# Kernel tuning notes

Measured on AMD Instinct MI355X. Metric: run time of the kernel, lower is better.

## Reference

```python
import jax, jax.numpy as jnp
import numpy as np

T, B, C, K, E = 1024, 32, 1024, 1024, 16  # seq, batch, d_model(=in=out), key_dim, n_experts
LOSS_SCALE = 0.01


def setup_inputs() -> dict:
    key0 = jax.random.key(0)
    k0, k1, k2, k3 = jax.random.split(key0, 4)
    x = jax.random.normal(k0, (T, B, C), dtype=jnp.float32)
    key = jax.random.normal(k1, (1, B, K), dtype=jnp.float32)
    bnd = float(np.sqrt(6.0 / (K + E)))  # xavier_uniform for assign Linear
    assign_w = jax.random.uniform(k2, (K, E), jnp.float32, -bnd, bnd)
    assign_b = jnp.zeros((E,), jnp.float32)
    a = float(np.sqrt(6.0) / (C + C))  # dynamic_init_method=1
    pw_w1 = jax.random.uniform(k3, (E, C * C), jnp.float32, -a, a)
    return {"x": x, "key": key, "assign_w": assign_w, "assign_b": assign_b, "pw_w1": pw_w1}


def reference(x, key, assign_w, assign_b, pw_w1):
    Tn, Bn, Cn = x.shape
    Tr = key.shape[0]  # key is provided -> Tr = 1 (one routing decision per batch element)
    En = assign_b.shape[0]
    # routing: softmax over experts (gumbel_tau=0 -> plain softmax branch)
    logits = key.reshape(Tr * Bn, -1) @ assign_w + assign_b  # (Tr*B, E)
    resp = jax.nn.softmax(logits, axis=-1)
    importance = resp.sum(axis=0)  # (E,)
    loss = LOSS_SCALE * jnp.std(importance, ddof=1) / jnp.mean(importance)  # torch.std is unbiased
    # mix expert weights: (Tr*B, E) @ (E, O*I) -> per-token/sentence weight matrix
    w = (resp @ pw_w1).reshape(Tr, Bn, Cn, Cn)  # (Tr, B, O, I)
    # batched matvec, broadcasting Tr=1 over T (sum over size-1 axis r == broadcast)
    y = jnp.einsum('rboi,tbi->tbo', w, x)
    return x + y, loss
```

## Files before the change

### kernel.cpp

```cpp
#include <hip/hip_runtime.h>
#include <stdint.h>


#define TBC   (1024*32*1024)

typedef __attribute__((ext_vector_type(8))) __bf16 bf16x8;
typedef __attribute__((ext_vector_type(4))) float  floatx4;

#define XSWZ(r) ((((r) & 3) ^ (((r) >> 2) & 3)))

__device__ __forceinline__ unsigned short f2bf(float f) {
  unsigned u = __float_as_uint(f);
  unsigned r = u + 0x7fffu + ((u >> 16) & 1u);
  return (unsigned short)(r >> 16);
}
__device__ __forceinline__ float bf2f(unsigned short u) {
  return __uint_as_float(((unsigned)u) << 16);
}

__device__ __forceinline__ void async16(const void* g, void* l) {
  __builtin_amdgcn_global_load_lds(
      (const __attribute__((address_space(1))) void*)(unsigned long long)(uintptr_t)g,
      (__attribute__((address_space(3))) void*)(unsigned int)(uintptr_t)l,
      16, 0, 0);
}

__global__ __launch_bounds__(256) void route_conv_kernel(
    const float* __restrict__ key, const float* __restrict__ aw,
    const float* __restrict__ ab, float* __restrict__ resp,
    const float4* __restrict__ x, ushort4* __restrict__ xb) {
  const int tid = threadIdx.x;
  if (blockIdx.x >= 32) {
    const int i0 = (blockIdx.x - 32) * 256 + tid;
    #pragma unroll
    for (int j = 0; j < 8; ++j) {
      const int i = i0 + j * 1048576;
      float4 v = x[i];
      ushort4 o;
      o.x = f2bf(v.x); o.y = f2bf(v.y); o.z = f2bf(v.z); o.w = f2bf(v.w);
      xb[i] = o;
    }
    return;
  }
  __shared__ float part[16][17];
  __shared__ float logit[16];
  const int b = blockIdx.x;
  const int e = tid & 15, ks = tid >> 4;
  const float* kb = key + b * 1024 + ks * 64;
  float acc = 0.f;
  #pragma unroll 8
  for (int k = 0; k < 64; ++k)
    acc = fmaf(kb[k], aw[(ks * 64 + k) * 16 + e], acc);
  part[e][ks] = acc;
  __syncthreads();
  if (tid < 16) {
    float s = ab[tid];
    #pragma unroll
    for (int j = 0; j < 16; ++j) s += part[tid][j];
    logit[tid] = s;
  }
  __syncthreads();
  if (tid < 16) {
    float m = logit[0];
    #pragma unroll
    for (int j = 1; j < 16; ++j) m = fmaxf(m, logit[j]);
    float s = 0.f;
    #pragma unroll
    for (int j = 0; j < 16; ++j) s += expf(logit[j] - m);
    resp[b * 16 + tid] = expf(logit[tid] - m) / s;
  }
}

__global__ __launch_bounds__(256, 4) void mix_loss_kernel(
    const float4* __restrict__ pw, const float* __restrict__ resp,
    ushort4* __restrict__ W, float* __restrict__ loss_out) {
  __shared__ float rs[512];
  const int tid = threadIdx.x;
  rs[tid] = resp[tid];
  rs[tid + 256] = resp[tid + 256];
  __syncthreads();
  if (blockIdx.x == 0 && tid == 0) {
    float imp[16];
    float mu = 0.f;
    #pragma unroll
    for (int e = 0; e < 16; ++e) {
      float s = 0.f;
      for (int bb = 0; bb < 32; ++bb) s += rs[bb * 16 + e];
      imp[e] = s; mu += s;
    }
    mu *= (1.f / 16.f);
    float var = 0.f;
    #pragma unroll
    for (int e = 0; e < 16; ++e) { float d = imp[e] - mu; var += d * d; }
    var *= (1.f / 15.f);
    loss_out[0] = 0.01f * sqrtf(var) / mu;
  }
  const int p = blockIdx.x * 256 + tid;
  float4 v[16];
  #pragma unroll
  for (int e = 0; e < 16; ++e) v[e] = pw[e * 262144 + p];
  #pragma unroll
  for (int b = 0; b < 32; ++b) {
    float ax = 0.f, ay = 0.f, az = 0.f, aww = 0.f;
    #pragma unroll
    for (int e = 0; e < 16; ++e) {
      const float r = rs[b * 16 + e];
      ax = fmaf(r, v[e].x, ax); ay = fmaf(r, v[e].y, ay);
      az = fmaf(r, v[e].z, az); aww = fmaf(r, v[e].w, aww);
    }
    ushort4 o;
    o.x = f2bf(ax); o.y = f2bf(ay); o.z = f2bf(az); o.w = f2bf(aww);
    W[(size_t)b * 262144 + p] = o;
  }
}

__global__ __launch_bounds__(512, 2) void gemm_kernel(
    const unsigned short* __restrict__ xb,
    const unsigned short* __restrict__ Wb,
    float* __restrict__ out) {
  __shared__ unsigned short lds[4][2][8192];
  const int tid  = threadIdx.x;
  const int lane = tid & 63;
  const int wave = tid >> 6;
  const int wm = wave >> 2;
  const int wn = wave & 3;

  const int gid   = blockIdx.x;
  const int xcd   = gid & 7;
  const int local = gid >> 3;
  const int b     = xcd * 4 + (local >> 4);
  const int sub   = local & 15;
  const int t0    = (sub >> 2) * 256;
  const int o0    = (sub & 3) * 256;

  const unsigned short* gA[2];
  const unsigned short* gB[2];
  #pragma unroll
  for (int j = 0; j < 2; ++j) {
    const int s  = j * 512 + tid;
    const int r  = s >> 2;
    const int cg = (s & 3) ^ XSWZ(r);
    gA[j] = xb + (size_t)(t0 + r) * 32768 + (size_t)b * 1024 + cg * 8;
    gB[j] = Wb + (size_t)b * 1048576 + (size_t)(o0 + r) * 1024 + cg * 8;
  }

  floatx4 acc[8][4];
  #pragma unroll
  for (int a = 0; a < 8; ++a)
    #pragma unroll
    for (int ni = 0; ni < 4; ++ni)
      acc[a][ni] = floatx4{0.f, 0.f, 0.f, 0.f};

  auto stage = [&](int bufi) {
    #pragma unroll
    for (int j = 0; j < 2; ++j) {
      const int dst = (j * 512 + wave * 64) * 8;
      async16(gA[j], &lds[bufi][0][dst]);
      async16(gB[j], &lds[bufi][1][dst]);
      gA[j] += 32; gB[j] += 32;
    }
  };

  auto compute = [&](int bufi) {
    const unsigned short* lA = &lds[bufi][0][0];
    const unsigned short* lB = &lds[bufi][1][0];
    bf16x8 bfr[4];
    #pragma unroll
    for (int ni = 0; ni < 4; ++ni) {
      const int r = wn * 64 + ni * 16 + (lane & 15);
      const int slot = (lane >> 4) ^ XSWZ(r);
      bfr[ni] = *(const bf16x8*)(lB + r * 32 + slot * 8);
    }
    #pragma unroll
    for (int half = 0; half < 2; ++half) {
      bf16x8 afr[4];
      #pragma unroll
      for (int mi = 0; mi < 4; ++mi) {
        const int r = wm * 128 + half * 64 + mi * 16 + (lane & 15);
        const int slot = (lane >> 4) ^ XSWZ(r);
        afr[mi] = *(const bf16x8*)(lA + r * 32 + slot * 8);
      }
      __builtin_amdgcn_s_setprio(1);
      #pragma unroll
      for (int mi = 0; mi < 4; ++mi)
        #pragma unroll
        for (int ni = 0; ni < 4; ++ni)
          acc[half * 4 + mi][ni] = __builtin_amdgcn_mfma_f32_16x16x32_bf16(
              afr[mi], bfr[ni], acc[half * 4 + mi][ni], 0, 0, 0);
      __builtin_amdgcn_s_setprio(0);
      if (half == 0) __builtin_amdgcn_s_barrier();
    }
  };

  stage(0); stage(1); stage(2);

  for (int t = 0; t < 32; ++t) {
    if (t <= 28) {
      stage((t + 3) & 3);
      asm volatile("s_waitcnt vmcnt(12)" ::: "memory");
    } else if (t == 29) {
      asm volatile("s_waitcnt vmcnt(8)" ::: "memory");
    } else if (t == 30) {
      asm volatile("s_waitcnt vmcnt(4)" ::: "memory");
    } else {
      asm volatile("s_waitcnt vmcnt(0)" ::: "memory");
    }
    __builtin_amdgcn_s_barrier();
    asm volatile("" ::: "memory");
    compute(t & 3);
    asm volatile("s_waitcnt lgkmcnt(0)" ::: "memory");
    __builtin_amdgcn_s_barrier();
  }

  #pragma unroll
  for (int a = 0; a < 8; ++a) {
    const int tb = t0 + wm * 128 + (a >> 2) * 64 + (a & 3) * 16 + (lane >> 4) * 4;
    #pragma unroll
    for (int ni = 0; ni < 4; ++ni) {
      const int o = o0 + wn * 64 + ni * 16 + (lane & 15);
      #pragma unroll
      for (int v = 0; v < 4; ++v) {
        const size_t idx = (size_t)(tb + v) * 32768 + (size_t)b * 1024 + o;
        out[idx] = acc[a][ni][v] + bf2f(xb[idx]);
      }
    }
  }
}

extern "C" void kernel_launch(void* const* d_in, const int* in_sizes, int n_in,
                              void* d_out, int out_size, void* d_ws, size_t ws_size,
                              hipStream_t stream) {
  const float* x   = (const float*)d_in[0];
  const float* key = (const float*)d_in[1];
  const float* aw  = (const float*)d_in[2];
  const float* ab  = (const float*)d_in[3];
  const float* pw  = (const float*)d_in[4];
  float* out = (float*)d_out;

  char* ws = (char*)d_ws;
  unsigned short* Wb = (unsigned short*)ws;
  unsigned short* xb = (unsigned short*)(ws + 67108864);
  float* resp        = (float*)(ws + 134217728);

  route_conv_kernel<<<4128, 256, 0, stream>>>(key, aw, ab, resp,
                                              (const float4*)x, (ushort4*)xb);
  mix_loss_kernel<<<1024, 256, 0, stream>>>((const float4*)pw, resp,
                                            (ushort4*)Wb, out + TBC);
  gemm_kernel<<<512, 512, 0, stream>>>(xb, Wb, out);
}
```

Measured before the change: 402.9 us.

## Switch GEMM to BK=64 double-buffered pipeline with 8-way XOR swizzle

The GEMM K-tile grows from 32 to 64, and the pipeline goes from four 32-wide stages to two 64-wide buffers. That halves the number of loop iterations and barriers, drops the mid-compute barrier, and uses a new 8-slot XOR swizzle for the wider LDS rows. The conversion kernel now processes contiguous chunks of 4 float4 per thread over twice as many blocks. The mix kernel's launch bounds are relaxed to allow more registers. The cost is a shallower prefetch depth, which can expose more memory latency per iteration.

```diff
diff --git a/kernel.cpp b/kernel.cpp
--- a/kernel.cpp
+++ b/kernel.cpp
@@ -6,8 +6,6 @@
 
 typedef __attribute__((ext_vector_type(8))) __bf16 bf16x8;
 typedef __attribute__((ext_vector_type(4))) float  floatx4;
-
-#define XSWZ(r) ((((r) & 3) ^ (((r) >> 2) & 3)))
 
 __device__ __forceinline__ unsigned short f2bf(float f) {
   unsigned u = __float_as_uint(f);
@@ -31,10 +29,10 @@
     const float4* __restrict__ x, ushort4* __restrict__ xb) {
   const int tid = threadIdx.x;
   if (blockIdx.x >= 32) {
-    const int i0 = (blockIdx.x - 32) * 256 + tid;
-    #pragma unroll
-    for (int j = 0; j < 8; ++j) {
-      const int i = i0 + j * 1048576;
+    const int base = (blockIdx.x - 32) * 1024 + tid;
+    #pragma unroll
+    for (int j = 0; j < 4; ++j) {
+      const int i = base + j * 256;
       float4 v = x[i];
       ushort4 o;
       o.x = f2bf(v.x); o.y = f2bf(v.y); o.z = f2bf(v.z); o.w = f2bf(v.w);
@@ -71,7 +69,7 @@
   }
 }
 
-__global__ __launch_bounds__(256, 4) void mix_loss_kernel(
+__global__ __launch_bounds__(256, 2) void mix_loss_kernel(
     const float4* __restrict__ pw, const float* __restrict__ resp,
     ushort4* __restrict__ W, float* __restrict__ loss_out) {
   __shared__ float rs[512];
@@ -118,9 +116,11 @@
     const unsigned short* __restrict__ xb,
     const unsigned short* __restrict__ Wb,
     float* __restrict__ out) {
-  __shared__ unsigned short lds[4][2][8192];
+  __shared__ unsigned short lds[65536];
   const int tid  = threadIdx.x;
   const int lane = tid & 63;
+  const int ln15 = lane & 15;
+  const int hi   = lane >> 4;
   const int wave = tid >> 6;
   const int wm = wave >> 2;
   const int wn = wave & 3;
@@ -133,16 +133,17 @@
   const int t0    = (sub >> 2) * 256;
   const int o0    = (sub & 3) * 256;
 
-  const unsigned short* gA[2];
-  const unsigned short* gB[2];
-  #pragma unroll
-  for (int j = 0; j < 2; ++j) {
-    const int s  = j * 512 + tid;
-    const int r  = s >> 2;
-    const int cg = (s & 3) ^ XSWZ(r);
-    gA[j] = xb + (size_t)(t0 + r) * 32768 + (size_t)b * 1024 + cg * 8;
-    gB[j] = Wb + (size_t)b * 1048576 + (size_t)(o0 + r) * 1024 + cg * 8;
-  }
+  const unsigned short* src[2][2][2];
+  #pragma unroll
+  for (int h = 0; h < 2; ++h)
+    #pragma unroll
+    for (int s = 0; s < 2; ++s) {
+      const int G  = tid + 512 * s;
+      const int r  = G >> 3;
+      const int kg = (G & 7) ^ (r & 7);
+      src[0][h][s] = xb + (size_t)(t0 + h * 128 + r) * 32768 + (size_t)b * 1024 + kg * 8;
+      src[1][h][s] = Wb + (size_t)b * 1048576 + (size_t)(o0 + h * 128 + r) * 1024 + kg * 8;
+    }
 
   floatx4 acc[8][4];
   #pragma unroll
@@ -151,77 +152,76 @@
     for (int ni = 0; ni < 4; ++ni)
       acc[a][ni] = floatx4{0.f, 0.f, 0.f, 0.f};
 
-  auto stage = [&](int bufi) {
-    #pragma unroll
-    for (int j = 0; j < 2; ++j) {
-      const int dst = (j * 512 + wave * 64) * 8;
-      async16(gA[j], &lds[bufi][0][dst]);
-      async16(gB[j], &lds[bufi][1][dst]);
-      gA[j] += 32; gB[j] += 32;
-    }
+  auto stage = [&](int bufBase) {
+    #pragma unroll
+    for (int ab = 0; ab < 2; ++ab)
+      #pragma unroll
+      for (int h = 0; h < 2; ++h)
+        #pragma unroll
+        for (int s = 0; s < 2; ++s) {
+          async16(src[ab][h][s],
+                  lds + bufBase + ab * 16384 + h * 8192 + (wave * 64 + 512 * s) * 8);
+          src[ab][h][s] += 64;
+        }
   };
 
-  auto compute = [&](int bufi) {
-    const unsigned short* lA = &lds[bufi][0][0];
-    const unsigned short* lB = &lds[bufi][1][0];
-    bf16x8 bfr[4];
+  auto compute = [&](int bufBase) {
+    const unsigned short* LA = lds + bufBase + wm * 8192;
+    const unsigned short* LB = lds + bufBase + 16384 + (wn >> 1) * 8192;
+    bf16x8 Bf[4][2];
     #pragma unroll
     for (int ni = 0; ni < 4; ++ni) {
-      const int r = wn * 64 + ni * 16 + (lane & 15);
-      const int slot = (lane >> 4) ^ XSWZ(r);
-      bfr[ni] = *(const bf16x8*)(lB + r * 32 + slot * 8);
-    }
-    #pragma unroll
-    for (int half = 0; half < 2; ++half) {
-      bf16x8 afr[4];
+      const int r = (wn & 1) * 64 + ni * 16 + ln15;
+      #pragma unroll
+      for (int kk = 0; kk < 2; ++kk)
+        Bf[ni][kk] = *(const bf16x8*)(LB + r * 64 + (((kk * 4 + hi) ^ (r & 7)) * 8));
+    }
+    #pragma unroll
+    for (int qm = 0; qm < 2; ++qm) {
+      bf16x8 Af[4][2];
       #pragma unroll
       for (int mi = 0; mi < 4; ++mi) {
-        const int r = wm * 128 + half * 64 + mi * 16 + (lane & 15);
-        const int slot = (lane >> 4) ^ XSWZ(r);
-        afr[mi] = *(const bf16x8*)(lA + r * 32 + slot * 8);
+        const int r = (qm * 4 + mi) * 16 + ln15;
+        #pragma unroll
+        for (int kk = 0; kk < 2; ++kk)
+          Af[mi][kk] = *(const bf16x8*)(LA + r * 64 + (((kk * 4 + hi) ^ (r & 7)) * 8));
       }
       __builtin_amdgcn_s_setprio(1);
       #pragma unroll
       for (int mi = 0; mi < 4; ++mi)
         #pragma unroll
         for (int ni = 0; ni < 4; ++ni)
-          acc[half * 4 + mi][ni] = __builtin_amdgcn_mfma_f32_16x16x32_bf16(
-              afr[mi], bfr[ni], acc[half * 4 + mi][ni], 0, 0, 0);
+          #pragma unroll
+          for (int kk = 0; kk < 2; ++kk)
+            acc[qm * 4 + mi][ni] = __builtin_amdgcn_mfma_f32_16x16x32_bf16(
+                Af[mi][kk], Bf[ni][kk], acc[qm * 4 + mi][ni], 0, 0, 0);
       __builtin_amdgcn_s_setprio(0);
-      if (half == 0) __builtin_amdgcn_s_barrier();
     }
   };
 
-  stage(0); stage(1); stage(2);
-
-  for (int t = 0; t < 32; ++t) {
-    if (t <= 28) {
-      stage((t + 3) & 3);
-      asm volatile("s_waitcnt vmcnt(12)" ::: "memory");
-    } else if (t == 29) {
-      asm volatile("s_waitcnt vmcnt(8)" ::: "memory");
-    } else if (t == 30) {
-      asm volatile("s_waitcnt vmcnt(4)" ::: "memory");
-    } else {
-      asm volatile("s_waitcnt vmcnt(0)" ::: "memory");
-    }
+  stage(0);
+  stage(32768);
+
+  for (int j = 0; j < 16; ++j) {
+    if (j < 15) asm volatile("s_waitcnt vmcnt(8)" ::: "memory");
+    else        asm volatile("s_waitcnt vmcnt(0)" ::: "memory");
+    __builtin_amdgcn_s_barrier();
+    compute((j & 1) * 32768);
     __builtin_amdgcn_s_barrier();
     asm volatile("" ::: "memory");
-    compute(t & 3);
-    asm volatile("s_waitcnt lgkmcnt(0)" ::: "memory");
-    __builtin_amdgcn_s_barrier();
-  }
-
-  #pragma unroll
-  for (int a = 0; a < 8; ++a) {
-    const int tb = t0 + wm * 128 + (a >> 2) * 64 + (a & 3) * 16 + (lane >> 4) * 4;
+    if (j < 14) stage((j & 1) * 32768);
+  }
+
+  #pragma unroll
+  for (int mi = 0; mi < 8; ++mi) {
+    const int tb = t0 + wm * 128 + mi * 16 + hi * 4;
     #pragma unroll
     for (int ni = 0; ni < 4; ++ni) {
-      const int o = o0 + wn * 64 + ni * 16 + (lane & 15);
+      const int o = o0 + wn * 64 + ni * 16 + ln15;
       #pragma unroll
       for (int v = 0; v < 4; ++v) {
         const size_t idx = (size_t)(tb + v) * 32768 + (size_t)b * 1024 + o;
-        out[idx] = acc[a][ni][v] + bf2f(xb[idx]);
+        out[idx] = acc[mi][ni][v] + bf2f(xb[idx]);
       }
     }
   }
@@ -242,7 +242,7 @@
   unsigned short* xb = (unsigned short*)(ws + 67108864);
   float* resp        = (float*)(ws + 134217728);
 
-  route_conv_kernel<<<4128, 256, 0, stream>>>(key, aw, ab, resp,
+  route_conv_kernel<<<8224, 256, 0, stream>>>(key, aw, ab, resp,
                                               (const float4*)x, (ushort4*)xb);
   mix_loss_kernel<<<1024, 256, 0, stream>>>((const float4*)pw, resp,
                                             (ushort4*)Wb, out + TBC);
```

Measured after the change: 381.0 us. 5.4% less time.
